# Performance work log

Measured on AMD Instinct MI355X. Metric: run time of the kernel, lower is better.

## Reference

```python
import jax, jax.numpy as jnp
import numpy as np

N_NODES = 50000
N_EDGES = 640000
IN_FEAT = 128
H_FEAT = 128
OUT_FEAT = 128
N_CLASSES = 16
BN_EPS = 1e-5


def gcn_conv(x, W, b, edge_index, n_nodes):
    """PyG GCNConv: add self-loops, symmetric deg^{-1/2} normalization,
    gather -> weighted message -> scatter_add, plus bias."""
    loop = jnp.arange(n_nodes, dtype=edge_index.dtype)
    src = jnp.concatenate([edge_index[0], loop])  # [E+N]
    dst = jnp.concatenate([edge_index[1], loop])  # [E+N]
    ones = jnp.ones(src.shape[0], dtype=x.dtype)
    deg = jax.ops.segment_sum(ones, dst, num_segments=n_nodes)  # >=1 (self loops)
    dinv = jax.lax.rsqrt(deg)
    norm = dinv[src] * dinv[dst]  # [E+N]
    h = x @ W  # [N, F_out]
    msgs = h[src] * norm[:, None]  # gather + scale, [E+N, F_out]
    out = jax.ops.segment_sum(msgs, dst, num_segments=n_nodes)  # scatter_add
    return out + b


def setup_inputs() -> dict:
    key = jax.random.key(0)
    ks = jax.random.split(key, 10)
    seq = jax.random.normal(ks[0], (N_NODES, IN_FEAT), dtype=jnp.float32)
    edge_index = jax.random.randint(ks[1], (2, N_EDGES), 0, N_NODES, dtype=jnp.int64)
    s1 = 1.0 / np.sqrt(IN_FEAT)
    s2 = 1.0 / np.sqrt(H_FEAT)
    s3 = 1.0 / np.sqrt(OUT_FEAT)
    W1 = jax.random.uniform(ks[2], (IN_FEAT, H_FEAT), jnp.float32, -s1, s1)
    b1 = jnp.zeros((H_FEAT,), jnp.float32)
    gamma = jnp.ones((H_FEAT,), jnp.float32)
    beta = jnp.zeros((H_FEAT,), jnp.float32)
    running_mean = 0.1 * jax.random.normal(ks[3], (H_FEAT,), jnp.float32)
    running_var = jax.random.uniform(ks[4], (H_FEAT,), jnp.float32, 0.5, 1.5)
    W2 = jax.random.uniform(ks[5], (H_FEAT, OUT_FEAT), jnp.float32, -s2, s2)
    b2 = jnp.zeros((OUT_FEAT,), jnp.float32)
    Wc = jax.random.uniform(ks[6], (OUT_FEAT, N_CLASSES), jnp.float32, -s3, s3)
    bc = jax.random.uniform(ks[7], (N_CLASSES,), jnp.float32, -s3, s3)
    return {
        "seq": seq, "edge_index": edge_index,
        "W1": W1, "b1": b1, "gamma": gamma, "beta": beta,
        "running_mean": running_mean, "running_var": running_var,
        "W2": W2, "b2": b2, "Wc": Wc, "bc": bc,
    }


def reference(seq, edge_index, W1, b1, gamma, beta, running_mean, running_var, W2, b2, Wc, bc):
    # inference mode: BN uses running stats, dropout is identity
    n = seq.shape[0]
    h = gcn_conv(seq, W1, b1, edge_index, n)
    h = (h - running_mean) * jax.lax.rsqrt(running_var + BN_EPS) * gamma + beta
    h = jax.nn.relu(h)
    h = gcn_conv(h, W2, b2, edge_index, n)
    return h @ Wc + bc
```

## Files before the change

kernel.cpp:

```cpp
#include <hip/hip_runtime.h>
#include <math.h>

#define N_NODES 50000
#define N_EDGES 640000
#define FDIM 128
#define NCLS 16
#define BN_EPS 1e-5f
#define NBS 196
#define NBG 782

__device__ __forceinline__ unsigned pack_bf16x2(float lo, float hi) {
    unsigned ul = __float_as_uint(lo);
    unsigned uh = __float_as_uint(hi);
    ul += 0x7fff + ((ul >> 16) & 1);
    uh += 0x7fff + ((uh >> 16) & 1);
    return (ul >> 16) | (uh & 0xffff0000u);
}
__device__ __forceinline__ float bf_lo(unsigned u) { return __uint_as_float(u << 16); }
__device__ __forceinline__ float bf_hi(unsigned u) { return __uint_as_float(u & 0xffff0000u); }

__global__ __launch_bounds__(256) void gemm_count_fold_kernel(
        const float* __restrict__ seq, const float* __restrict__ W1,
        unsigned* __restrict__ bufA,
        const int* __restrict__ eidx, int* __restrict__ deg,
        const float* __restrict__ W2, const float* __restrict__ Wc,
        const float* __restrict__ b1, const float* __restrict__ b2,
        const float* __restrict__ bc, const float* __restrict__ gamma,
        const float* __restrict__ beta, const float* __restrict__ rmean,
        const float* __restrict__ rvar,
        float* __restrict__ W2c, float* __restrict__ bc2, float4* __restrict__ fusedq) {
    __shared__ __align__(16) char smem[24832];
    int tid = threadIdx.x;
    int bid = blockIdx.x;

    if (bid < NBG) {
        float* sX = (float*)smem;
        float* sW = (float*)(smem + 64 * 33 * 4);
        float4* sW4 = (float4*)sW;
        int r0 = bid * 64;
        int colg = tid & 15, rowt = tid >> 4;
        float acc[4][8];
#pragma unroll
        for (int i = 0; i < 4; i++)
#pragma unroll
            for (int j = 0; j < 8; j++) acc[i][j] = 0.f;
        const float4* X4 = (const float4*)seq;
        const float4* W4 = (const float4*)W1;
#pragma unroll
        for (int kt = 0; kt < 4; kt++) {
#pragma unroll
            for (int i = 0; i < 2; i++) {
                int idx = tid + i * 256;
                int row = idx >> 3, k4 = idx & 7;
                float4 v = make_float4(0.f, 0.f, 0.f, 0.f);
                if (r0 + row < N_NODES) v = X4[(size_t)(r0 + row) * 32 + kt * 8 + k4];
                float* p = &sX[row * 33 + k4 * 4];
                p[0] = v.x; p[1] = v.y; p[2] = v.z; p[3] = v.w;
            }
#pragma unroll
            for (int i = 0; i < 4; i++) {
                int idx = tid + i * 256;
                int kk = idx >> 5, c4 = idx & 31;
                sW4[kk * 32 + c4] = W4[(size_t)(kt * 32 + kk) * 32 + c4];
            }
            __syncthreads();
#pragma unroll 8
            for (int k = 0; k < 32; k++) {
                float4 w0 = sW4[k * 32 + colg * 2];
                float4 w1 = sW4[k * 32 + colg * 2 + 1];
                float xs[4];
#pragma unroll
                for (int i = 0; i < 4; i++) xs[i] = sX[(rowt * 4 + i) * 33 + k];
#pragma unroll
                for (int i = 0; i < 4; i++) {
                    acc[i][0] += xs[i] * w0.x; acc[i][1] += xs[i] * w0.y;
                    acc[i][2] += xs[i] * w0.z; acc[i][3] += xs[i] * w0.w;
                    acc[i][4] += xs[i] * w1.x; acc[i][5] += xs[i] * w1.y;
                    acc[i][6] += xs[i] * w1.z; acc[i][7] += xs[i] * w1.w;
                }
            }
            __syncthreads();
        }
#pragma unroll
        for (int i = 0; i < 4; i++) {
            int row = r0 + rowt * 4 + i;
            if (row < N_NODES) {
                uint4 pv;
                pv.x = pack_bf16x2(acc[i][0], acc[i][1]);
                pv.y = pack_bf16x2(acc[i][2], acc[i][3]);
                pv.z = pack_bf16x2(acc[i][4], acc[i][5]);
                pv.w = pack_bf16x2(acc[i][6], acc[i][7]);
                *((uint4*)(bufA + (size_t)row * 64 + colg * 4)) = pv;
            }
        }
    } else if (bid < NBG + 625) {
        const int4* dst4 = (const int4*)(eidx + N_EDGES);
        int t = (bid - NBG) * 256 + tid;
        int4 d = dst4[t];
        atomicAdd(&deg[d.x], 1);
        atomicAdd(&deg[d.y], 1);
        atomicAdd(&deg[d.z], 1);
        atomicAdd(&deg[d.w], 1);
    } else {
        int fb = bid - (NBG + 625);
        int gid = fb * 256 + tid;
        int r = gid >> 4, c = gid & 15;
        float acc = 0.f;
#pragma unroll 8
        for (int k = 0; k < 128; k++) acc += W2[r * 128 + k] * Wc[k * 16 + c];
        W2c[gid] = acc;
        if (fb == 0) {
            if (tid < 16) {
                float a = bc[tid];
                for (int k = 0; k < 128; k++) a += b2[k] * Wc[k * 16 + tid];
                bc2[tid] = a;
            }
            if (tid < 64) {
                int c0 = tid * 2, c1 = c0 + 1;
                float sc0 = gamma[c0] * rsqrtf(rvar[c0] + BN_EPS);
                float sc1 = gamma[c1] * rsqrtf(rvar[c1] + BN_EPS);
                float sh0 = (b1[c0] - rmean[c0]) * sc0 + beta[c0];
                float sh1 = (b1[c1] - rmean[c1]) * sc1 + beta[c1];
                fusedq[tid] = make_float4(sc0, sh0, sc1, sh1);
            }
        }
    }
}

__global__ __launch_bounds__(256) void scan_kernel(const int* __restrict__ deg,
                                                   int* __restrict__ offs,
                                                   int* __restrict__ partials,
                                                   float* __restrict__ dinv,
                                                   int* __restrict__ cursor,
                                                   int* __restrict__ done) {
    __shared__ int s[256];
    __shared__ int isLast;
    int tid = threadIdx.x;
    int gid = blockIdx.x * 256 + tid;
    int v = (gid < N_NODES) ? deg[gid] : 0;
    if (gid < N_NODES) {
        dinv[gid] = rsqrtf((float)(v + 1));
        cursor[gid] = 0;
    }
    s[tid] = v;
    __syncthreads();
    for (int off = 1; off < 256; off <<= 1) {
        int t2 = (tid >= off) ? s[tid - off] : 0;
        __syncthreads();
        s[tid] += t2;
        __syncthreads();
    }
    if (gid <= N_NODES) offs[gid] = s[tid] - v;
    if (tid == 255) partials[blockIdx.x] = s[255];

    __threadfence();
    if (tid == 0) isLast = (atomicAdd(done, 1) == NBS - 1);
    __syncthreads();
    if (isLast) {
        __threadfence();
        int pv = (tid < NBS) ? partials[tid] : 0;
        s[tid] = pv;
        __syncthreads();
        for (int off = 1; off < 256; off <<= 1) {
            int t2 = (tid >= off) ? s[tid - off] : 0;
            __syncthreads();
            s[tid] += t2;
            __syncthreads();
        }
        if (tid < NBS) partials[tid] = s[tid] - pv;
    }
}

__global__ __launch_bounds__(256) void fill_csr_kernel(const int* __restrict__ eidx,
                                                       const int* __restrict__ offs,
                                                       const int* __restrict__ part,
                                                       const float* __restrict__ dinv,
                                                       int* __restrict__ cursor,
                                                       int2* __restrict__ csr_sw) {
    const int4* src4 = (const int4*)eidx;
    const int4* dst4 = (const int4*)(eidx + N_EDGES);
    int t = blockIdx.x * 256 + threadIdx.x;
    int4 sv = src4[t];
    int4 dv = dst4[t];
    {
        int pos = offs[dv.x] + part[dv.x >> 8] + atomicAdd(&cursor[dv.x], 1);
        csr_sw[pos] = make_int2(sv.x, __float_as_int(dinv[sv.x]));
    }
    {
        int pos = offs[dv.y] + part[dv.y >> 8] + atomicAdd(&cursor[dv.y], 1);
        csr_sw[pos] = make_int2(sv.y, __float_as_int(dinv[sv.y]));
    }
    {
        int pos = offs[dv.z] + part[dv.z >> 8] + atomicAdd(&cursor[dv.z], 1);
        csr_sw[pos] = make_int2(sv.z, __float_as_int(dinv[sv.z]));
    }
    {
        int pos = offs[dv.w] + part[dv.w >> 8] + atomicAdd(&cursor[dv.w], 1);
        csr_sw[pos] = make_int2(sv.w, __float_as_int(dinv[sv.w]));
    }
}

__global__ __launch_bounds__(256) void agg1_kernel(const unsigned* __restrict__ Hb,
                                                   const int2* __restrict__ csr_sw,
                                                   const int* __restrict__ offs,
                                                   const int* __restrict__ part,
                                                   const float* __restrict__ dinv,
                                                   const float4* __restrict__ fusedq,
                                                   const float* __restrict__ W2c,
                                                   float* __restrict__ Z) {
    __shared__ float sH[4][128];
    int w = threadIdx.x >> 6, l = threadIdx.x & 63;
    int node = blockIdx.x * 4 + w;
    int beg = __builtin_amdgcn_readfirstlane(offs[node] + part[node >> 8]);
    int end = __builtin_amdgcn_readfirstlane(offs[node + 1] + part[(node + 1) >> 8]);
    float di = dinv[node];

    int c = l & 15, q = l >> 4;
    float wreg[32];
#pragma unroll
    for (int i = 0; i < 32; i++) wreg[i] = W2c[(q * 32 + i) * 16 + c];

    unsigned hv = Hb[(size_t)node * 64 + l];
    float n2 = di * di;
    float acc0 = bf_lo(hv) * n2, acc1 = bf_hi(hv) * n2;

    int e = beg;
    for (; e + 8 <= end; e += 8) {
        int2 a0 = csr_sw[e];     int2 a1 = csr_sw[e + 1];
        int2 a2 = csr_sw[e + 2]; int2 a3 = csr_sw[e + 3];
        int2 a4 = csr_sw[e + 4]; int2 a5 = csr_sw[e + 5];
        int2 a6 = csr_sw[e + 6]; int2 a7 = csr_sw[e + 7];
        unsigned u0 = Hb[(size_t)a0.x * 64 + l];
        unsigned u1 = Hb[(size_t)a1.x * 64 + l];
        unsigned u2 = Hb[(size_t)a2.x * 64 + l];
        unsigned u3 = Hb[(size_t)a3.x * 64 + l];
        unsigned u4 = Hb[(size_t)a4.x * 64 + l];
        unsigned u5 = Hb[(size_t)a5.x * 64 + l];
        unsigned u6 = Hb[(size_t)a6.x * 64 + l];
        unsigned u7 = Hb[(size_t)a7.x * 64 + l];
        float w0 = __int_as_float(a0.y) * di, w1 = __int_as_float(a1.y) * di;
        float w2 = __int_as_float(a2.y) * di, w3 = __int_as_float(a3.y) * di;
        float w4 = __int_as_float(a4.y) * di, w5 = __int_as_float(a5.y) * di;
        float w6 = __int_as_float(a6.y) * di, w7 = __int_as_float(a7.y) * di;
        acc0 += bf_lo(u0) * w0 + bf_lo(u1) * w1 + bf_lo(u2) * w2 + bf_lo(u3) * w3
              + bf_lo(u4) * w4 + bf_lo(u5) * w5 + bf_lo(u6) * w6 + bf_lo(u7) * w7;
        acc1 += bf_hi(u0) * w0 + bf_hi(u1) * w1 + bf_hi(u2) * w2 + bf_hi(u3) * w3
              + bf_hi(u4) * w4 + bf_hi(u5) * w5 + bf_hi(u6) * w6 + bf_hi(u7) * w7;
    }
    while (e < end) {
        int i1 = e + 1 < end ? e + 1 : end - 1;
        int i2 = e + 2 < end ? e + 2 : end - 1;
        int i3 = e + 3 < end ? e + 3 : end - 1;
        int2 a0 = csr_sw[e];  int2 a1 = csr_sw[i1];
        int2 a2 = csr_sw[i2]; int2 a3 = csr_sw[i3];
        unsigned u0 = Hb[(size_t)a0.x * 64 + l];
        unsigned u1 = Hb[(size_t)a1.x * 64 + l];
        unsigned u2 = Hb[(size_t)a2.x * 64 + l];
        unsigned u3 = Hb[(size_t)a3.x * 64 + l];
        float w0 = __int_as_float(a0.y) * di;
        float w1 = (e + 1 < end) ? __int_as_float(a1.y) * di : 0.f;
        float w2 = (e + 2 < end) ? __int_as_float(a2.y) * di : 0.f;
        float w3 = (e + 3 < end) ? __int_as_float(a3.y) * di : 0.f;
        acc0 += bf_lo(u0) * w0 + bf_lo(u1) * w1 + bf_lo(u2) * w2 + bf_lo(u3) * w3;
        acc1 += bf_hi(u0) * w0 + bf_hi(u1) * w1 + bf_hi(u2) * w2 + bf_hi(u3) * w3;
        e += 4;
    }

    float4 qv = fusedq[l];
    float a0 = fmaxf(acc0 * qv.x + qv.y, 0.f);
    float a1 = fmaxf(acc1 * qv.z + qv.w, 0.f);

    ((float2*)sH[w])[l] = make_float2(a0, a1);
    float z = 0.f;
    const float4* row4 = (const float4*)&sH[w][q * 32];
#pragma unroll
    for (int i = 0; i < 8; i++) {
        float4 v = row4[i];
        z += v.x * wreg[i * 4] + v.y * wreg[i * 4 + 1]
           + v.z * wreg[i * 4 + 2] + v.w * wreg[i * 4 + 3];
    }
    z += __shfl_xor(z, 16);
    z += __shfl_xor(z, 32);
    if (l < 16) Z[(size_t)node * NCLS + l] = z;
}

__global__ __launch_bounds__(256) void agg2_kernel(const float* __restrict__ Z,
                                                   const int2* __restrict__ csr_sw,
                                                   const int* __restrict__ offs,
                                                   const int* __restrict__ part,
                                                   const float* __restrict__ dinv,
                                                   const float* __restrict__ bc2,
                                                   float* __restrict__ out) {
    int grp = threadIdx.x >> 4, c = threadIdx.x & 15;
    int node = blockIdx.x * 16 + grp;
    int beg = offs[node] + part[node >> 8];
    int end = offs[node + 1] + part[(node + 1) >> 8];
    float di = dinv[node];

    float acc = Z[(size_t)node * NCLS + c] * di * di;
    int e = beg;
    for (; e + 8 <= end; e += 8) {
        int2 a0 = csr_sw[e],     a1 = csr_sw[e + 1];
        int2 a2 = csr_sw[e + 2], a3 = csr_sw[e + 3];
        int2 a4 = csr_sw[e + 4], a5 = csr_sw[e + 5];
        int2 a6 = csr_sw[e + 6], a7 = csr_sw[e + 7];
        float v0 = Z[(size_t)a0.x * NCLS + c];
        float v1 = Z[(size_t)a1.x * NCLS + c];
        float v2 = Z[(size_t)a2.x * NCLS + c];
        float v3 = Z[(size_t)a3.x * NCLS + c];
        float v4 = Z[(size_t)a4.x * NCLS + c];
        float v5 = Z[(size_t)a5.x * NCLS + c];
        float v6 = Z[(size_t)a6.x * NCLS + c];
        float v7 = Z[(size_t)a7.x * NCLS + c];
        acc += v0 * (__int_as_float(a0.y) * di) + v1 * (__int_as_float(a1.y) * di)
             + v2 * (__int_as_float(a2.y) * di) + v3 * (__int_as_float(a3.y) * di)
             + v4 * (__int_as_float(a4.y) * di) + v5 * (__int_as_float(a5.y) * di)
             + v6 * (__int_as_float(a6.y) * di) + v7 * (__int_as_float(a7.y) * di);
    }
    for (; e < end; e++) {
        int2 a = csr_sw[e];
        acc += Z[(size_t)a.x * NCLS + c] * (__int_as_float(a.y) * di);
    }
    out[(size_t)node * NCLS + c] = acc + bc2[c];
}

extern "C" void kernel_launch(void* const* d_in, const int* in_sizes, int n_in,
                              void* d_out, int out_size, void* d_ws, size_t ws_size,
                              hipStream_t stream) {
    const float* seq   = (const float*)d_in[0];
    const int*   eidx  = (const int*)d_in[1];
    const float* W1    = (const float*)d_in[2];
    const float* b1    = (const float*)d_in[3];
    const float* gamma = (const float*)d_in[4];
    const float* beta  = (const float*)d_in[5];
    const float* rmean = (const float*)d_in[6];
    const float* rvar  = (const float*)d_in[7];
    const float* W2    = (const float*)d_in[8];
    const float* b2    = (const float*)d_in[9];
    const float* Wc    = (const float*)d_in[10];
    const float* bc    = (const float*)d_in[11];

    char* ws = (char*)d_ws;
    size_t off = 0;
    auto alloc = [&](size_t bytes) -> void* {
        void* p = ws + off;
        off = (off + bytes + 255) & ~(size_t)255;
        return p;
    };
    int*    ctl      = (int*)alloc(256);
    int*    deg      = (int*)alloc(N_NODES * 4);
    int*    cursor   = (int*)alloc(N_NODES * 4);
    int*    offs     = (int*)alloc((N_NODES + 1) * 4);
    int*    partials = (int*)alloc(256 * 4);
    float*  dinv     = (float*)alloc(N_NODES * 4);
    int2*   csr_sw   = (int2*)alloc((size_t)N_EDGES * 8);
    float*  W2c      = (float*)alloc(FDIM * NCLS * 4);
    float*  bc2      = (float*)alloc(NCLS * 4);
    float4* fusedq   = (float4*)alloc(64 * 16);
    unsigned* bufA   = (unsigned*)alloc((size_t)N_NODES * (FDIM / 2) * 4);
    float*  Zbuf     = (float*)alloc((size_t)N_NODES * NCLS * 4);

    hipMemsetAsync(ctl, 0, 256 + (size_t)N_NODES * 4, stream);
    gemm_count_fold_kernel<<<NBG + 625 + 8, 256, 0, stream>>>(
        seq, W1, bufA, eidx, deg, W2, Wc, b1, b2, bc, gamma, beta, rmean, rvar,
        W2c, bc2, fusedq);
    scan_kernel<<<NBS, 256, 0, stream>>>(deg, offs, partials, dinv, cursor, ctl);
    fill_csr_kernel<<<625, 256, 0, stream>>>(eidx, offs, partials, dinv, cursor, csr_sw);
    agg1_kernel<<<N_NODES / 4, 256, 0, stream>>>(bufA, csr_sw, offs, partials,
                                                 dinv, fusedq, W2c, Zbuf);
    agg2_kernel<<<N_NODES / 16, 256, 0, stream>>>(Zbuf, csr_sw, offs, partials,
                                                  dinv, bc2, (float*)d_out);
}
```

Baseline: 230.8 us.

## Compute first-layer GEMM with split-bf16 MFMA instead of scalar FMA

The seq @ W1 tile is moved from scalar FP32 FMAs over shared-memory tiles onto 16x16x32 bf16 matrix-core instructions. Both operands are split into high and low bf16 parts, and three MFMAs per step approximate fp32 accuracy. W1 fragments are pre-split into 64KB of LDS per block, and results are staged through LDS for coalesced bf16 stores. Each of the 782 blocks redundantly converts all of W1, and the larger LDS footprint lowers occupancy for the other roles that share this fused kernel.

```diff
diff --git a/kernel.cpp b/kernel.cpp
--- a/kernel.cpp
+++ b/kernel.cpp
@@ -9,12 +9,20 @@
 #define NBS 196
 #define NBG 782
 
+typedef __attribute__((ext_vector_type(8))) short bf16x8;
+typedef __attribute__((ext_vector_type(4))) float f32x4;
+
 __device__ __forceinline__ unsigned pack_bf16x2(float lo, float hi) {
     unsigned ul = __float_as_uint(lo);
     unsigned uh = __float_as_uint(hi);
     ul += 0x7fff + ((ul >> 16) & 1);
     uh += 0x7fff + ((uh >> 16) & 1);
     return (ul >> 16) | (uh & 0xffff0000u);
+}
+__device__ __forceinline__ unsigned short bf16_rne(float x) {
+    unsigned u = __float_as_uint(x);
+    u += 0x7fff + ((u >> 16) & 1);
+    return (unsigned short)(u >> 16);
 }
 __device__ __forceinline__ float bf_lo(unsigned u) { return __uint_as_float(u << 16); }
 __device__ __forceinline__ float bf_hi(unsigned u) { return __uint_as_float(u & 0xffff0000u); }
@@ -29,69 +37,99 @@
         const float* __restrict__ beta, const float* __restrict__ rmean,
         const float* __restrict__ rvar,
         float* __restrict__ W2c, float* __restrict__ bc2, float4* __restrict__ fusedq) {
-    __shared__ __align__(16) char smem[24832];
+    __shared__ __align__(16) char smem[65536];
     int tid = threadIdx.x;
     int bid = blockIdx.x;
 
     if (bid < NBG) {
-        float* sX = (float*)smem;
-        float* sW = (float*)(smem + 64 * 33 * 4);
-        float4* sW4 = (float4*)sW;
+        bf16x8* WH = (bf16x8*)smem;
+        bf16x8* WL = (bf16x8*)(smem + 32768);
+        {
+            int f0 = tid * 8;
+#pragma unroll
+            for (int fo = 0; fo < 8; fo++) {
+                int fi = f0 + fo;
+                int lane = fi & 63, kt = (fi >> 6) & 3, ct = fi >> 8;
+                int kbase = kt * 32 + (lane >> 4) * 8;
+                int col = ct * 16 + (lane & 15);
+                short h[8], lo[8];
+#pragma unroll
+                for (int j = 0; j < 8; j++) {
+                    float wv = W1[(kbase + j) * 128 + col];
+                    unsigned short hs = bf16_rne(wv);
+                    float rem = wv - __uint_as_float(((unsigned)hs) << 16);
+                    h[j] = (short)hs;
+                    lo[j] = (short)bf16_rne(rem);
+                }
+                WH[fi] = *(bf16x8*)h;
+                WL[fi] = *(bf16x8*)lo;
+            }
+        }
+        __syncthreads();
+
+        int w = tid >> 6, l = tid & 63;
+        int la = l & 15, q = l >> 4;
         int r0 = bid * 64;
-        int colg = tid & 15, rowt = tid >> 4;
-        float acc[4][8];
-#pragma unroll
-        for (int i = 0; i < 4; i++)
-#pragma unroll
-            for (int j = 0; j < 8; j++) acc[i][j] = 0.f;
+        int arow = r0 + w * 16 + la;
+        bool rowok = arow < N_NODES;
         const float4* X4 = (const float4*)seq;
-        const float4* W4 = (const float4*)W1;
+
+        float4 xr[8];
 #pragma unroll
         for (int kt = 0; kt < 4; kt++) {
-#pragma unroll
-            for (int i = 0; i < 2; i++) {
-                int idx = tid + i * 256;
-                int row = idx >> 3, k4 = idx & 7;
-                float4 v = make_float4(0.f, 0.f, 0.f, 0.f);
-                if (r0 + row < N_NODES) v = X4[(size_t)(r0 + row) * 32 + kt * 8 + k4];
-                float* p = &sX[row * 33 + k4 * 4];
-                p[0] = v.x; p[1] = v.y; p[2] = v.z; p[3] = v.w;
+            float4 z4 = make_float4(0.f, 0.f, 0.f, 0.f);
+            xr[kt * 2]     = rowok ? X4[arow * 32 + kt * 8 + q * 2]     : z4;
+            xr[kt * 2 + 1] = rowok ? X4[arow * 32 + kt * 8 + q * 2 + 1] : z4;
+        }
+        bf16x8 ah[4], al[4];
+#pragma unroll
+        for (int kt = 0; kt < 4; kt++) {
+            const float* xv = (const float*)&xr[kt * 2];
+#pragma unroll
+            for (int j = 0; j < 8; j++) {
+                float v = xv[j];
+                unsigned short hs = bf16_rne(v);
+                float rem = v - __uint_as_float(((unsigned)hs) << 16);
+                ah[kt][j] = (short)hs;
+                al[kt][j] = (short)bf16_rne(rem);
             }
-#pragma unroll
-            for (int i = 0; i < 4; i++) {
-                int idx = tid + i * 256;
-                int kk = idx >> 5, c4 = idx & 31;
-                sW4[kk * 32 + c4] = W4[(size_t)(kt * 32 + kk) * 32 + c4];
+        }
+        f32x4 acc[8];
+#pragma unroll
+        for (int ct = 0; ct < 8; ct++) acc[ct] = (f32x4){0.f, 0.f, 0.f, 0.f};
+
+#pragma unroll
+        for (int kt = 0; kt < 4; kt++) {
+#pragma unroll
+            for (int ct = 0; ct < 8; ct++) {
+                bf16x8 bh = WH[(ct * 4 + kt) * 64 + l];
+                bf16x8 bl = WL[(ct * 4 + kt) * 64 + l];
+                acc[ct] = __builtin_amdgcn_mfma_f32_16x16x32_bf16(ah[kt], bh, acc[ct], 0, 0, 0);
+                acc[ct] = __builtin_amdgcn_mfma_f32_16x16x32_bf16(ah[kt], bl, acc[ct], 0, 0, 0);
+                acc[ct] = __builtin_amdgcn_mfma_f32_16x16x32_bf16(al[kt], bh, acc[ct], 0, 0, 0);
             }
-            __syncthreads();
-#pragma unroll 8
-            for (int k = 0; k < 32; k++) {
-                float4 w0 = sW4[k * 32 + colg * 2];
-                float4 w1 = sW4[k * 32 + colg * 2 + 1];
-                float xs[4];
-#pragma unroll
-                for (int i = 0; i < 4; i++) xs[i] = sX[(rowt * 4 + i) * 33 + k];
-#pragma unroll
-                for (int i = 0; i < 4; i++) {
-                    acc[i][0] += xs[i] * w0.x; acc[i][1] += xs[i] * w0.y;
-                    acc[i][2] += xs[i] * w0.z; acc[i][3] += xs[i] * w0.w;
-                    acc[i][4] += xs[i] * w1.x; acc[i][5] += xs[i] * w1.y;
-                    acc[i][6] += xs[i] * w1.z; acc[i][7] += xs[i] * w1.w;
-                }
-            }
-            __syncthreads();
-        }
-#pragma unroll
-        for (int i = 0; i < 4; i++) {
-            int row = r0 + rowt * 4 + i;
-            if (row < N_NODES) {
-                uint4 pv;
-                pv.x = pack_bf16x2(acc[i][0], acc[i][1]);
-                pv.y = pack_bf16x2(acc[i][2], acc[i][3]);
-                pv.z = pack_bf16x2(acc[i][4], acc[i][5]);
-                pv.w = pack_bf16x2(acc[i][6], acc[i][7]);
-                *((uint4*)(bufA + (size_t)row * 64 + colg * 4)) = pv;
-            }
+        }
+        __syncthreads();
+
+        float* sC = (float*)smem;
+#pragma unroll
+        for (int ct = 0; ct < 8; ct++)
+#pragma unroll
+            for (int r = 0; r < 4; r++)
+                sC[(w * 16 + q * 4 + r) * 132 + ct * 16 + la] = acc[ct][r];
+        __syncthreads();
+
+        int trow = tid >> 2, tcb = (tid & 3) * 32;
+        int grow = r0 + trow;
+        if (grow < N_NODES) {
+            const float* sr = sC + trow * 132 + tcb;
+            unsigned ob[16];
+#pragma unroll
+            for (int t = 0; t < 16; t++) ob[t] = pack_bf16x2(sr[2 * t], sr[2 * t + 1]);
+            uint4* dp = (uint4*)(bufA + (size_t)grow * 64 + (tid & 3) * 16);
+#pragma unroll
+            for (int g = 0; g < 4; g++)
+                dp[g] = make_uint4(ob[g * 4], ob[g * 4 + 1], ob[g * 4 + 2], ob[g * 4 + 3]);
         }
     } else if (bid < NBG + 625) {
         const int4* dst4 = (const int4*)(eidx + N_EDGES);
```

New measurement: 229.2 us. No clear change (-0.7%).
